# Kernel optimization log

Hardware: AMD Instinct MI355X
Metric: run time of the kernel (lower is better)

## Reference

```python
import jax, jax.numpy as jnp
import numpy as np

D_MODEL = 2048
NUM_HEADS = 16
NUM_KV_HEADS = 4
D_HEAD = D_MODEL // NUM_HEADS  # 128
GROUPS = NUM_HEADS // NUM_KV_HEADS  # 4
ROPE_THETA = 10000.0
EPS = 1e-6


def setup_inputs() -> dict:
    key = jax.random.key(0)
    ks = jax.random.split(key, 7)
    B, S = 2, 2048
    s = 1.0 / np.sqrt(D_MODEL)
    return {
        "qkv": jax.random.normal(ks[0], (B, S, D_MODEL), dtype=jnp.float32),
        "Wq": jax.random.normal(ks[1], (D_MODEL, D_MODEL), dtype=jnp.float32) * s,
        "Wk": jax.random.normal(ks[2], (NUM_KV_HEADS * D_HEAD, D_MODEL), dtype=jnp.float32) * s,
        "Wv": jax.random.normal(ks[3], (NUM_KV_HEADS * D_HEAD, D_MODEL), dtype=jnp.float32) * s,
        "Wo": jax.random.normal(ks[4], (D_MODEL, D_MODEL), dtype=jnp.float32) * s,
        "q_gamma": jnp.ones((D_HEAD,), dtype=jnp.float32),
        "k_gamma": jnp.ones((D_HEAD,), dtype=jnp.float32),
    }


def _rmsnorm(x, gamma):
    # per-head RMSNorm over last dim (d_head)
    var = jnp.mean(jnp.square(x), axis=-1, keepdims=True)
    return x * jax.lax.rsqrt(var + EPS) * gamma


def _rope(x, cos, sin):
    # x: [B, S, H, Dh]; cos/sin: [S, Dh]
    half = x.shape[-1] // 2
    x1, x2 = x[..., :half], x[..., half:]
    rot = jnp.concatenate([-x2, x1], axis=-1)
    return x * cos[None, :, None, :] + rot * sin[None, :, None, :]


def reference(qkv, Wq, Wk, Wv, Wo, q_gamma, k_gamma):
    B, S, D = qkv.shape
    q = jnp.einsum("bsd,ed->bse", qkv, Wq).reshape(B, S, NUM_HEADS, D_HEAD)
    k = jnp.einsum("bsd,ed->bse", qkv, Wk).reshape(B, S, NUM_KV_HEADS, D_HEAD)
    v = jnp.einsum("bsd,ed->bse", qkv, Wv).reshape(B, S, NUM_KV_HEADS, D_HEAD)

    q = _rmsnorm(q, q_gamma)
    k = _rmsnorm(k, k_gamma)

    # RoPE, position_ids = arange(S)
    pos = jnp.arange(S, dtype=jnp.float32)
    inv_freq = 1.0 / (ROPE_THETA ** (jnp.arange(0, D_HEAD, 2, dtype=jnp.float32) / D_HEAD))
    ang = pos[:, None] * inv_freq[None, :]                 # [S, Dh/2]
    cos = jnp.concatenate([jnp.cos(ang), jnp.cos(ang)], axis=-1)  # [S, Dh]
    sin = jnp.concatenate([jnp.sin(ang), jnp.sin(ang)], axis=-1)
    q = _rope(q, cos, sin)
    k = _rope(k, cos, sin)

    # [B, H, S, Dh]
    q = q.transpose(0, 2, 1, 3)
    k = k.transpose(0, 2, 1, 3)
    v = v.transpose(0, 2, 1, 3)
    # GQA: repeat kv heads
    k = jnp.repeat(k, GROUPS, axis=1)
    v = jnp.repeat(v, GROUPS, axis=1)

    scale = 1.0 / np.sqrt(D_HEAD)
    scores = jnp.einsum("bhqd,bhkd->bhqk", q, k) * scale
    causal = jnp.tril(jnp.ones((S, S), dtype=bool))
    scores = jnp.where(causal[None, None], scores, jnp.finfo(scores.dtype).min)
    probs = jax.nn.softmax(scores, axis=-1)
    attended = jnp.einsum("bhqk,bhkd->bhqd", probs, v)     # [B, H, S, Dh]
    attended = attended.transpose(0, 2, 1, 3).reshape(B, S, D)
    return jnp.einsum("bsd,ed->bse", attended, Wo)
```

## Files before the change

kernel.cpp:

```cpp
#include <hip/hip_runtime.h>

#define S_LEN 2048
#define B_SZ 2
#define DMODEL 2048
#define NHEADS 16
#define NKV 4
#define DHEAD 128
#define SCALE 0.08838834764831845f
#define KVB 32

typedef __bf16 bf16x8 __attribute__((ext_vector_type(8)));
typedef __bf16 bf16x4 __attribute__((ext_vector_type(4)));
typedef float f32x4 __attribute__((ext_vector_type(4)));

#define MFMA(a, b, c) __builtin_amdgcn_mfma_f32_16x16x32_bf16(a, b, c, 0, 0, 0)

__device__ __forceinline__ void gload_lds16(const __bf16* g, __bf16* l) {
    __builtin_amdgcn_global_load_lds(
        (const __attribute__((address_space(1))) unsigned int*)g,
        (__attribute__((address_space(3))) unsigned int*)l, 16, 0, 0);
}

__global__ void rope_tables_kernel(float* __restrict__ cosT, float* __restrict__ sinT) {
    int i = blockIdx.x * 256 + threadIdx.x;
    int s = i >> 6, d = i & 63;
    float freq = powf(10000.0f, -(2.0f * (float)d) / 128.0f);
    float ang = (float)s * freq;
    cosT[i] = cosf(ang);
    sinT[i] = sinf(ang);
}

__global__ __launch_bounds__(256) void convert_kernel(
    const float* __restrict__ s0, const float* __restrict__ s1,
    const float* __restrict__ s2, const float* __restrict__ s3,
    const float* __restrict__ s4,
    __bf16* __restrict__ d0, __bf16* __restrict__ d1, __bf16* __restrict__ d2,
    __bf16* __restrict__ d3, __bf16* __restrict__ d4) {
    const float* s;
    __bf16* d;
    int n8;
    switch (blockIdx.y) {
        case 0: s = s0; d = d0; n8 = (B_SZ * S_LEN * DMODEL) / 8; break;
        case 1: s = s1; d = d1; n8 = (DMODEL * DMODEL) / 8; break;
        case 2: s = s2; d = d2; n8 = (NKV * DHEAD * DMODEL) / 8; break;
        case 3: s = s3; d = d3; n8 = (NKV * DHEAD * DMODEL) / 8; break;
        default: s = s4; d = d4; n8 = (DMODEL * DMODEL) / 8; break;
    }
    for (int i = blockIdx.x * 256 + threadIdx.x; i < n8; i += 512 * 256) {
        float4 a = ((const float4*)s)[2 * i];
        float4 b = ((const float4*)s)[2 * i + 1];
        bf16x8 o = {(__bf16)a.x, (__bf16)a.y, (__bf16)a.z, (__bf16)a.w,
                    (__bf16)b.x, (__bf16)b.y, (__bf16)b.z, (__bf16)b.w};
        *(bf16x8*)&d[i * 8] = o;
    }
}

template <int BM>
__device__ __forceinline__ void gemm256(const __bf16* __restrict__ A,
                                        const __bf16* __restrict__ W,
                                        int bm, int bn, int K,
                                        f32x4 (&acc)[BM / 32][4]) {
    constexpr int MI = BM / 32;
    constexpr int ALT = BM / 64;
    __shared__ alignas(16) __bf16 As[2][BM * 64];
    __shared__ alignas(16) __bf16 Bs[2][256 * 64];
    const int tid = threadIdx.x;
    const int lane = tid & 63;
    const int wave = tid >> 6;
    const int lr = lane & 15, lk = lane >> 4;
    const int wr = wave >> 2;
    const int wc = wave & 3;
    const int sRow = lane >> 3;
    const int sCol = 8 * ((lane & 7) ^ sRow);

    auto stageA = [&](int bi, int k0) {
#pragma unroll
        for (int it = 0; it < ALT; ++it) {
            const int row = it * 64 + wave * 8 + sRow;
            gload_lds16(A + (size_t)(bm + row) * K + k0 + sCol,
                        &As[bi][it * 4096 + wave * 512]);
        }
    };
    auto stageB = [&](int bi, int k0) {
#pragma unroll
        for (int it = 0; it < 4; ++it) {
            const int row = it * 64 + wave * 8 + sRow;
            gload_lds16(W + (size_t)(bn + row) * K + k0 + sCol,
                        &Bs[bi][it * 4096 + wave * 512]);
        }
    };

#pragma unroll
    for (int mi = 0; mi < MI; ++mi)
#pragma unroll
        for (int ni = 0; ni < 4; ++ni) acc[mi][ni] = (f32x4){0.f, 0.f, 0.f, 0.f};

    const int NT = K >> 6;
    stageA(0, 0);
    stageB(0, 0);
    stageA(1, 64);
    stageB(1, 64);
    if constexpr (BM == 256) asm volatile("s_waitcnt vmcnt(8)" ::: "memory");
    else                     asm volatile("s_waitcnt vmcnt(6)" ::: "memory");
    __builtin_amdgcn_s_barrier();

    for (int t = 0; t < NT; ++t) {
        const int bi = t & 1;
#pragma unroll
        for (int kk = 0; kk < 2; ++kk) {
            bf16x8 af[MI], bfr[4];
#pragma unroll
            for (int i = 0; i < MI; ++i) {
                const int r = wr * (BM / 2) + i * 16 + lr;
                const int slot = (kk * 4 + lk) ^ (r & 7);
                af[i] = *(const bf16x8*)&As[bi][r * 64 + slot * 8];
            }
#pragma unroll
            for (int i = 0; i < 4; ++i) {
                const int r = wc * 64 + i * 16 + lr;
                const int slot = (kk * 4 + lk) ^ (r & 7);
                bfr[i] = *(const bf16x8*)&Bs[bi][r * 64 + slot * 8];
            }
#pragma unroll
            for (int mi = 0; mi < MI; ++mi)
#pragma unroll
                for (int ni = 0; ni < 4; ++ni)
                    acc[mi][ni] = MFMA(af[mi], bfr[ni], acc[mi][ni]);
        }
        asm volatile("s_waitcnt lgkmcnt(0)" ::: "memory");
        __builtin_amdgcn_sched_barrier(0);
        __builtin_amdgcn_s_barrier();
        if (t + 2 < NT) {
            stageA(bi, (t + 2) * 64);
            stageB(bi, (t + 2) * 64);
        }
        if (t + 1 < NT) {
            if (t + 2 < NT) {
                if constexpr (BM == 256) asm volatile("s_waitcnt vmcnt(8)" ::: "memory");
                else                     asm volatile("s_waitcnt vmcnt(6)" ::: "memory");
            } else {
                asm volatile("s_waitcnt vmcnt(0)" ::: "memory");
            }
            __builtin_amdgcn_s_barrier();
        }
    }
}

__global__ __launch_bounds__(512, 2) void qkv_proj_kernel(
    const __bf16* __restrict__ qkvb, const __bf16* __restrict__ Wq,
    const __bf16* __restrict__ Wk, const __bf16* __restrict__ Wv,
    float* __restrict__ q_tmp, float* __restrict__ k_tmp, float* __restrict__ v_tmp) {
    const int id = (blockIdx.x & 7) * 24 + (blockIdx.x >> 3);
    const int bmi = id / 12, bni = id % 12;
    const int bm = bmi * 256;
    const __bf16* W;
    float* C;
    int ldc, bn;
    if (bni < 8)       { W = Wq; C = q_tmp; ldc = 2048; bn = bni * 256; }
    else if (bni < 10) { W = Wk; C = k_tmp; ldc = 512;  bn = (bni - 8) * 256; }
    else               { W = Wv; C = v_tmp; ldc = 512;  bn = (bni - 10) * 256; }

    f32x4 acc[8][4];
    gemm256<256>(qkvb, W, bm, bn, 2048, acc);

    const int lane = threadIdx.x & 63, wave = threadIdx.x >> 6;
    const int lr = lane & 15, lk = lane >> 4;
    const int wr = wave >> 2, wc = wave & 3;
#pragma unroll
    for (int mi = 0; mi < 8; ++mi)
#pragma unroll
        for (int ni = 0; ni < 4; ++ni)
#pragma unroll
            for (int r = 0; r < 4; ++r) {
                const int row = bm + wr * 128 + mi * 16 + lk * 4 + r;
                const int col = bn + wc * 64 + ni * 16 + lr;
                C[(size_t)row * ldc + col] = acc[mi][ni][r];
            }
}

__global__ __launch_bounds__(512, 2) void out_proj_kernel(
    const __bf16* __restrict__ att, const __bf16* __restrict__ Wo,
    float* __restrict__ out) {
    const int id = (blockIdx.x & 7) * 32 + (blockIdx.x >> 3);
    const int bm = (id >> 3) * 128, bn = (id & 7) * 256;

    f32x4 acc[4][4];
    gemm256<128>(att, Wo, bm, bn, 2048, acc);

    const int lane = threadIdx.x & 63, wave = threadIdx.x >> 6;
    const int lr = lane & 15, lk = lane >> 4;
    const int wr = wave >> 2, wc = wave & 3;
#pragma unroll
    for (int mi = 0; mi < 4; ++mi)
#pragma unroll
        for (int ni = 0; ni < 4; ++ni)
#pragma unroll
            for (int r = 0; r < 4; ++r) {
                const int row = bm + wr * 64 + mi * 16 + lk * 4 + r;
                const int col = bn + wc * 64 + ni * 16 + lr;
                out[(size_t)row * DMODEL + col] = acc[mi][ni][r];
            }
}

__global__ __launch_bounds__(256) void postproc_kernel(
    const float* __restrict__ q_tmp, const float* __restrict__ k_tmp,
    const float* __restrict__ qg, const float* __restrict__ kg,
    const float* __restrict__ cosT, const float* __restrict__ sinT,
    __bf16* __restrict__ qb, __bf16* __restrict__ kb) {
    int bs = blockIdx.x;
    int b = bs >> 11, s = bs & 2047;
    int wave = threadIdx.x >> 6, lane = threadIdx.x & 63;
    float c  = cosT[s * 64 + lane];
    float sn = sinT[s * 64 + lane];
    float g1q = qg[lane], g2q = qg[lane + 64];
    float g1k = kg[lane], g2k = kg[lane + 64];

    for (int h = wave; h < NHEADS; h += 4) {
        const float* row = q_tmp + (size_t)bs * 2048 + h * 128;
        float x1 = row[lane], x2 = row[lane + 64];
        float ss = x1 * x1 + x2 * x2;
#pragma unroll
        for (int m = 1; m < 64; m <<= 1) ss += __shfl_xor(ss, m);
        float rs = rsqrtf(ss * (1.0f / 128.0f) + 1e-6f);
        float n1 = x1 * rs * g1q, n2 = x2 * rs * g2q;
        float y1 = (n1 * c - n2 * sn) * SCALE;
        float y2 = (n2 * c + n1 * sn) * SCALE;
        __bf16* orow = qb + (((size_t)(b * NHEADS + h)) * S_LEN + s) * DHEAD;
        orow[lane] = (__bf16)y1;
        orow[lane + 64] = (__bf16)y2;
    }
    int h = wave;
    if (h < NKV) {
        const float* row = k_tmp + (size_t)bs * 512 + h * 128;
        float x1 = row[lane], x2 = row[lane + 64];
        float ss = x1 * x1 + x2 * x2;
#pragma unroll
        for (int m = 1; m < 64; m <<= 1) ss += __shfl_xor(ss, m);
        float rs = rsqrtf(ss * (1.0f / 128.0f) + 1e-6f);
        float n1 = x1 * rs * g1k, n2 = x2 * rs * g2k;
        float y1 = n1 * c - n2 * sn;
        float y2 = n2 * c + n1 * sn;
        __bf16* orow = kb + (((size_t)(b * NKV + h)) * S_LEN + s) * DHEAD;
        orow[lane] = (__bf16)y1;
        orow[lane + 64] = (__bf16)y2;
    }
}

__global__ __launch_bounds__(256) void v_transpose_kernel(
    const float* __restrict__ v_tmp, __bf16* __restrict__ vt) {
    int bkv = blockIdx.x;
    int b = bkv >> 2, kvh = bkv & 3;
    int s0 = blockIdx.y * 64, d0 = blockIdx.z * 64;
    __shared__ float tile[64][65];
#pragma unroll
    for (int i = 0; i < 16; ++i) {
        int idx = threadIdx.x + i * 256;
        int r = idx >> 6, cc = idx & 63;
        tile[r][cc] = v_tmp[((size_t)(b * S_LEN) + s0 + r) * 512 + kvh * 128 + d0 + cc];
    }
    __syncthreads();
#pragma unroll
    for (int i = 0; i < 16; ++i) {
        int idx = threadIdx.x + i * 256;
        int r = idx >> 6, cc = idx & 63;
        vt[((size_t)bkv * DHEAD + d0 + r) * S_LEN + s0 + cc] = (__bf16)tile[cc][r];
    }
}

__global__ __launch_bounds__(256, 2) void flash_kernel(
    const __bf16* __restrict__ qb, const __bf16* __restrict__ kb,
    const __bf16* __restrict__ vt, __bf16* __restrict__ att) {
    __shared__ alignas(16) __bf16 K_lds[2][32 * 128];
    __shared__ alignas(16) __bf16 V_lds[2][128 * 32];
    __shared__ alignas(16) __bf16 p_lds[4][16][40];

    const int bh = blockIdx.x;
    const int b = bh >> 4, h = bh & 15, kv = h >> 2;
    const int j = blockIdx.y;
    const int lane = threadIdx.x & 63, wave = threadIdx.x >> 6;
    const int lr = lane & 15, lk = lane >> 4;

    const int qloB = j * 64 + wave * 16;
    const int qhiB = (31 - j) * 64 + wave * 16;
    const int ntL  = ((qloB + 15) >> 5) + 1;
    const int ntHw = ((qhiB + 15) >> 5) + 1;
    const int ntH  = 64 - 2 * j;

    const __bf16* Qp = qb + ((size_t)(b * NHEADS + h)) * S_LEN * DHEAD;
    const __bf16* Kp = kb + ((size_t)(b * NKV + kv)) * S_LEN * DHEAD;
    const __bf16* Vt = vt + ((size_t)(b * NKV + kv)) * DHEAD * S_LEN;

    bf16x8 qlo[4], qhi[4];
#pragma unroll
    for (int f = 0; f < 4; ++f) {
        qlo[f] = *(const bf16x8*)&Qp[(size_t)(qloB + lr) * DHEAD + f * 32 + lk * 8];
        qhi[f] = *(const bf16x8*)&Qp[(size_t)(qhiB + lr) * DHEAD + f * 32 + lk * 8];
    }

    const int c0 = 2 * wave;
    const int l4 = lane >> 4, l15 = lane & 15;
    const int l2 = lane >> 2, l3 = lane & 3;
    const int vcol = ((l3 ^ (l2 & 3)) << 3);

    auto stage = [&](int bufi, int t) {
        const int k0s = t * KVB;
#pragma unroll
        for (int i = 0; i < 2; ++i) {
            const int c = c0 + i;
            const int rK = c * 4 + l4;
            const int kcol = ((l15 ^ (rK & 7)) << 3);
            gload_lds16(Kp + (size_t)(k0s + rK) * DHEAD + kcol, &K_lds[bufi][c * 512]);
            const int rV = c * 16 + l2;
            gload_lds16(Vt + (size_t)rV * S_LEN + k0s + vcol, &V_lds[bufi][c * 512]);
        }
    };

    f32x4 accL[8] = {}, accH[8] = {};
    float lsumL[4] = {0.f, 0.f, 0.f, 0.f}, lsumH[4] = {0.f, 0.f, 0.f, 0.f};
    const int swzK = (lr & 7) << 4;
    const int swzV = (lr & 3) << 4;

    auto frag_step = [&](const bf16x8 (&qf)[4], int qbase, f32x4 (&acc)[8],
                         float (&lsum)[4], const bf16x8 (&kf)[8],
                         const bf16x8 (&vf)[8], int k0) {
        f32x4 sc[2] = {};
#pragma unroll
        for (int kk = 0; kk < 2; ++kk)
#pragma unroll
            for (int f = 0; f < 4; ++f)
                sc[kk] = MFMA(qf[f], kf[kk * 4 + f], sc[kk]);
        asm volatile("s_waitcnt lgkmcnt(0)" ::: "memory");
#pragma unroll
        for (int r = 0; r < 4; ++r) {
            const int qr = qbase + lk * 4 + r;
            float s0 = sc[0][r], s1 = sc[1][r];
            if (k0 + lr > qr) s0 = -1e30f;
            if (k0 + 16 + lr > qr) s1 = -1e30f;
            float p0 = __expf(s0), p1 = __expf(s1);
            lsum[r] += p0 + p1;
            p_lds[wave][lk * 4 + r][lr] = (__bf16)p0;
            p_lds[wave][lk * 4 + r][lr + 16] = (__bf16)p1;
        }
        asm volatile("s_waitcnt lgkmcnt(0)" ::: "memory");
        bf16x8 pf = *(const bf16x8*)&p_lds[wave][lr][lk * 8];
#pragma unroll
        for (int nf = 0; nf < 8; ++nf)
            acc[nf] = MFMA(pf, vf[nf], acc[nf]);
    };

    int cur = 0;
    stage(0, 0);
    __syncthreads();
    for (int t = 0; t < ntH; ++t) {
        if (t + 1 < ntH) stage(cur ^ 1, t + 1);
        const int k0 = t * KVB;
        bf16x8 kf[8], vf[8];
#pragma unroll
        for (int kk = 0; kk < 2; ++kk)
#pragma unroll
            for (int f = 0; f < 4; ++f) {
                const int cb = (f * 64 + lk * 16) ^ swzK;
                kf[kk * 4 + f] =
                    *(const bf16x8*)((const char*)&K_lds[cur][(kk * 16 + lr) * 128] + cb);
            }
#pragma unroll
        for (int nf = 0; nf < 8; ++nf) {
            const int cb = (lk * 16) ^ swzV;
            vf[nf] = *(const bf16x8*)((const char*)&V_lds[cur][(nf * 16 + lr) * 32] + cb);
        }
        if (t < ntHw) frag_step(qhi, qhiB, accH, lsumH, kf, vf, k0);
        if (t < ntL)  frag_step(qlo, qloB, accL, lsumL, kf, vf, k0);
        __syncthreads();
        cur ^= 1;
    }

#pragma unroll
    for (int r = 0; r < 4; ++r) {
#pragma unroll
        for (int m = 1; m < 16; m <<= 1) {
            lsumL[r] += __shfl_xor(lsumL[r], m);
            lsumH[r] += __shfl_xor(lsumH[r], m);
        }
    }
#pragma unroll
    for (int nf = 0; nf < 8; ++nf)
#pragma unroll
        for (int r = 0; r < 4; ++r) {
            int qrL = qloB + lk * 4 + r;
            int qrH = qhiB + lk * 4 + r;
            att[((size_t)(b * S_LEN) + qrL) * DMODEL + h * DHEAD + nf * 16 + lr] =
                (__bf16)(accL[nf][r] / lsumL[r]);
            att[((size_t)(b * S_LEN) + qrH) * DMODEL + h * DHEAD + nf * 16 + lr] =
                (__bf16)(accH[nf][r] / lsumH[r]);
        }
}

extern "C" void kernel_launch(void* const* d_in, const int* in_sizes, int n_in,
                              void* d_out, int out_size, void* d_ws, size_t ws_size,
                              hipStream_t stream) {
    const float* qkv = (const float*)d_in[0];
    const float* Wq  = (const float*)d_in[1];
    const float* Wk  = (const float*)d_in[2];
    const float* Wv  = (const float*)d_in[3];
    const float* Wo  = (const float*)d_in[4];
    const float* qg  = (const float*)d_in[5];
    const float* kg  = (const float*)d_in[6];
    float* out = (float*)d_out;

    size_t off = 0;
    char* wsb = (char*)d_ws;
    auto alloc = [&](size_t n) {
        char* p = wsb + off;
        off += (n + 255) & ~(size_t)255;
        return (void*)p;
    };
    const size_t M = (size_t)B_SZ * S_LEN;
    float* cosT  = (float*)alloc((size_t)S_LEN * 64 * 4);
    float* sinT  = (float*)alloc((size_t)S_LEN * 64 * 4);
    float* q_tmp = (float*)alloc(M * 2048 * 4);
    float* k_tmp = (float*)alloc(M * 512 * 4);
    float* v_tmp = (float*)alloc(M * 512 * 4);
    __bf16* qb   = (__bf16*)alloc((size_t)B_SZ * NHEADS * S_LEN * DHEAD * 2);
    __bf16* kb   = (__bf16*)alloc((size_t)B_SZ * NKV * S_LEN * DHEAD * 2);
    __bf16* vt   = (__bf16*)alloc((size_t)B_SZ * NKV * DHEAD * S_LEN * 2);
    __bf16* att  = (__bf16*)alloc(M * DMODEL * 2);
    __bf16* wo_b = (__bf16*)alloc((size_t)DMODEL * DMODEL * 2);
    __bf16* qkv_b = att;
    __bf16* wq_b  = qb;
    __bf16* wk_b  = vt;
    __bf16* wv_b  = wk_b + (size_t)NKV * DHEAD * DMODEL;

    rope_tables_kernel<<<(S_LEN * 64) / 256, 256, 0, stream>>>(cosT, sinT);
    convert_kernel<<<dim3(512, 5), 256, 0, stream>>>(qkv, Wq, Wk, Wv, Wo,
                                                     qkv_b, wq_b, wk_b, wv_b, wo_b);
    qkv_proj_kernel<<<192, 512, 0, stream>>>(qkv_b, wq_b, wk_b, wv_b,
                                             q_tmp, k_tmp, v_tmp);
    postproc_kernel<<<dim3(M), 256, 0, stream>>>(q_tmp, k_tmp, qg, kg, cosT, sinT, qb, kb);
    v_transpose_kernel<<<dim3(B_SZ * NKV, S_LEN / 64, DHEAD / 64), 256, 0, stream>>>(v_tmp, vt);
    flash_kernel<<<dim3(B_SZ * NHEADS, 16), 256, 0, stream>>>(qb, kb, vt, att);
    out_proj_kernel<<<256, 512, 0, stream>>>(att, wo_b, out);
}
```

Before: 211.5 us.

## Fuse RMSNorm, RoPE and V transpose into QKV projection epilogue

Measured after the change: 195.3 us. 7.6% less time.

```diff
diff --git a/kernel.cpp b/kernel.cpp
--- a/kernel.cpp
+++ b/kernel.cpp
@@ -59,11 +59,12 @@
 __device__ __forceinline__ void gemm256(const __bf16* __restrict__ A,
                                         const __bf16* __restrict__ W,
                                         int bm, int bn, int K,
-                                        f32x4 (&acc)[BM / 32][4]) {
+                                        f32x4 (&acc)[BM / 32][4],
+                                        __bf16* arena) {
     constexpr int MI = BM / 32;
     constexpr int ALT = BM / 64;
-    __shared__ alignas(16) __bf16 As[2][BM * 64];
-    __shared__ alignas(16) __bf16 Bs[2][256 * 64];
+    __bf16* As = arena;
+    __bf16* Bs = arena + 2 * BM * 64;
     const int tid = threadIdx.x;
     const int lane = tid & 63;
     const int wave = tid >> 6;
@@ -78,7 +79,7 @@
         for (int it = 0; it < ALT; ++it) {
             const int row = it * 64 + wave * 8 + sRow;
             gload_lds16(A + (size_t)(bm + row) * K + k0 + sCol,
-                        &As[bi][it * 4096 + wave * 512]);
+                        As + bi * BM * 64 + it * 4096 + wave * 512);
         }
     };
     auto stageB = [&](int bi, int k0) {
@@ -86,7 +87,7 @@
         for (int it = 0; it < 4; ++it) {
             const int row = it * 64 + wave * 8 + sRow;
             gload_lds16(W + (size_t)(bn + row) * K + k0 + sCol,
-                        &Bs[bi][it * 4096 + wave * 512]);
+                        Bs + bi * 16384 + it * 4096 + wave * 512);
         }
     };
 
@@ -113,13 +114,13 @@
             for (int i = 0; i < MI; ++i) {
                 const int r = wr * (BM / 2) + i * 16 + lr;
                 const int slot = (kk * 4 + lk) ^ (r & 7);
-                af[i] = *(const bf16x8*)&As[bi][r * 64 + slot * 8];
+                af[i] = *(const bf16x8*)&As[bi * BM * 64 + r * 64 + slot * 8];
             }
 #pragma unroll
             for (int i = 0; i < 4; ++i) {
                 const int r = wc * 64 + i * 16 + lr;
                 const int slot = (kk * 4 + lk) ^ (r & 7);
-                bfr[i] = *(const bf16x8*)&Bs[bi][r * 64 + slot * 8];
+                bfr[i] = *(const bf16x8*)&Bs[bi * 16384 + r * 64 + slot * 8];
             }
 #pragma unroll
             for (int mi = 0; mi < MI; ++mi)
@@ -149,43 +150,138 @@
 __global__ __launch_bounds__(512, 2) void qkv_proj_kernel(
     const __bf16* __restrict__ qkvb, const __bf16* __restrict__ Wq,
     const __bf16* __restrict__ Wk, const __bf16* __restrict__ Wv,
-    float* __restrict__ q_tmp, float* __restrict__ k_tmp, float* __restrict__ v_tmp) {
+    const float* __restrict__ qg, const float* __restrict__ kg,
+    const float* __restrict__ cosT, const float* __restrict__ sinT,
+    __bf16* __restrict__ qb, __bf16* __restrict__ kb, __bf16* __restrict__ vt) {
+    __shared__ alignas(16) __bf16 arena[4 * 256 * 64];
     const int id = (blockIdx.x & 7) * 24 + (blockIdx.x >> 3);
     const int bmi = id / 12, bni = id % 12;
     const int bm = bmi * 256;
     const __bf16* W;
-    float* C;
-    int ldc, bn;
-    if (bni < 8)       { W = Wq; C = q_tmp; ldc = 2048; bn = bni * 256; }
-    else if (bni < 10) { W = Wk; C = k_tmp; ldc = 512;  bn = (bni - 8) * 256; }
-    else               { W = Wv; C = v_tmp; ldc = 512;  bn = (bni - 10) * 256; }
+    int bn;
+    if (bni < 8)       { W = Wq; bn = bni * 256; }
+    else if (bni < 10) { W = Wk; bn = (bni - 8) * 256; }
+    else               { W = Wv; bn = (bni - 10) * 256; }
 
     f32x4 acc[8][4];
-    gemm256<256>(qkvb, W, bm, bn, 2048, acc);
-
-    const int lane = threadIdx.x & 63, wave = threadIdx.x >> 6;
+    gemm256<256>(qkvb, W, bm, bn, 2048, acc, arena);
+
+    const int tid = threadIdx.x;
+    const int lane = tid & 63, wave = tid >> 6;
     const int lr = lane & 15, lk = lane >> 4;
     const int wr = wave >> 2, wc = wave & 3;
-#pragma unroll
-    for (int mi = 0; mi < 8; ++mi)
-#pragma unroll
-        for (int ni = 0; ni < 4; ++ni)
+    const int dc0 = (wc & 1) * 64;
+
+    if (bni < 10) {
+        const bool isQ = (bni < 8);
+        const float* gamma = isQ ? qg : kg;
+        const float scl = isQ ? SCALE : 1.0f;
+        const int hh = (isQ ? bni * 2 : (bni - 8) * 2) + (wc >> 1);
+        const int nh = isQ ? NHEADS : NKV;
+        __bf16* outb = isQ ? qb : kb;
+        float g[4];
+#pragma unroll
+        for (int ni = 0; ni < 4; ++ni) g[ni] = gamma[dc0 + ni * 16 + lr];
+
+        float* xbuf = (float*)arena;
+        float* ssbuf = (float*)((char*)arena + 70 * 1024);
+
+        float rs[8][4];
+#pragma unroll
+        for (int mi = 0; mi < 8; ++mi)
 #pragma unroll
             for (int r = 0; r < 4; ++r) {
-                const int row = bm + wr * 128 + mi * 16 + lk * 4 + r;
-                const int col = bn + wc * 64 + ni * 16 + lr;
-                C[(size_t)row * ldc + col] = acc[mi][ni][r];
-            }
+                float ss = 0.f;
+#pragma unroll
+                for (int ni = 0; ni < 4; ++ni) ss += acc[mi][ni][r] * acc[mi][ni][r];
+                ss += __shfl_xor(ss, 1);
+                ss += __shfl_xor(ss, 2);
+                ss += __shfl_xor(ss, 4);
+                ss += __shfl_xor(ss, 8);
+                if (lr == 0) ssbuf[wc * 256 + wr * 128 + mi * 16 + lk * 4 + r] = ss;
+            }
+        __syncthreads();
+#pragma unroll
+        for (int mi = 0; mi < 8; ++mi)
+#pragma unroll
+            for (int r = 0; r < 4; ++r) {
+                const int rowl = wr * 128 + mi * 16 + lk * 4 + r;
+                const float tot = ssbuf[wc * 256 + rowl] + ssbuf[(wc ^ 1) * 256 + rowl];
+                rs[mi][r] = rsqrtf(tot * (1.0f / 128.0f) + 1e-6f) * scl;
+            }
+        __syncthreads();
+
+#pragma unroll
+        for (int ch = 0; ch < 4; ++ch) {
+            float y[2][4][4];
+#pragma unroll
+            for (int m2 = 0; m2 < 2; ++m2)
+#pragma unroll
+                for (int ni = 0; ni < 4; ++ni)
+#pragma unroll
+                    for (int r = 0; r < 4; ++r) {
+                        const int mi = ch * 2 + m2;
+                        y[m2][ni][r] = acc[mi][ni][r] * rs[mi][r] * g[ni];
+                        xbuf[tid * 33 + m2 * 16 + ni * 4 + r] = y[m2][ni][r];
+                    }
+            __syncthreads();
+            float yp[2][4][4];
+#pragma unroll
+            for (int m2 = 0; m2 < 2; ++m2)
+#pragma unroll
+                for (int ni = 0; ni < 4; ++ni)
+#pragma unroll
+                    for (int r = 0; r < 4; ++r)
+                        yp[m2][ni][r] = xbuf[(tid ^ 64) * 33 + m2 * 16 + ni * 4 + r];
+#pragma unroll
+            for (int m2 = 0; m2 < 2; ++m2)
+#pragma unroll
+                for (int r = 0; r < 4; ++r) {
+                    const int mi = ch * 2 + m2;
+                    const int gm = bm + wr * 128 + mi * 16 + lk * 4 + r;
+                    const int bb = gm >> 11, s = gm & 2047;
+                    const float* ct = cosT + s * 64;
+                    const float* st = sinT + s * 64;
+                    __bf16* orow = outb + (((size_t)(bb * nh + hh)) * S_LEN + s) * DHEAD;
+#pragma unroll
+                    for (int ni = 0; ni < 4; ++ni) {
+                        const int dd = ni * 16 + lr;
+                        const float c = ct[dd], sn = st[dd];
+                        const float own = y[m2][ni][r], par = yp[m2][ni][r];
+                        const float o = (wc & 1) ? (own * c + par * sn)
+                                                 : (own * c - par * sn);
+                        orow[dc0 + dd] = (__bf16)o;
+                    }
+                }
+            __syncthreads();
+        }
+    } else {
+        const int kvh = (bni - 10) * 2 + (wc >> 1);
+#pragma unroll
+        for (int mi = 0; mi < 8; ++mi) {
+            const int gm = bm + wr * 128 + mi * 16 + lk * 4;
+            const int bb = gm >> 11, s0 = gm & 2047;
+            __bf16* vbase = vt + ((size_t)(bb * NKV + kvh)) * DHEAD * S_LEN;
+#pragma unroll
+            for (int ni = 0; ni < 4; ++ni) {
+                const int d = dc0 + ni * 16 + lr;
+                bf16x4 pk = {(__bf16)acc[mi][ni][0], (__bf16)acc[mi][ni][1],
+                             (__bf16)acc[mi][ni][2], (__bf16)acc[mi][ni][3]};
+                *(bf16x4*)&vbase[(size_t)d * S_LEN + s0] = pk;
+            }
+        }
+    }
 }
 
 __global__ __launch_bounds__(512, 2) void out_proj_kernel(
     const __bf16* __restrict__ att, const __bf16* __restrict__ Wo,
     float* __restrict__ out) {
+    __shared__ alignas(16) __bf16 arena[2 * 128 * 64 + 2 * 256 * 64];
     const int id = (blockIdx.x & 7) * 32 + (blockIdx.x >> 3);
     const int bm = (id >> 3) * 128, bn = (id & 7) * 256;
 
     f32x4 acc[4][4];
-    gemm256<128>(att, Wo, bm, bn, 2048, acc);
+    gemm256<128>(att, Wo, bm, bn, 2048, acc, arena);
 
     const int lane = threadIdx.x & 63, wave = threadIdx.x >> 6;
     const int lr = lane & 15, lk = lane >> 4;
@@ -200,71 +296,6 @@
                 const int col = bn + wc * 64 + ni * 16 + lr;
                 out[(size_t)row * DMODEL + col] = acc[mi][ni][r];
             }
-}
-
-__global__ __launch_bounds__(256) void postproc_kernel(
-    const float* __restrict__ q_tmp, const float* __restrict__ k_tmp,
-    const float* __restrict__ qg, const float* __restrict__ kg,
-    const float* __restrict__ cosT, const float* __restrict__ sinT,
-    __bf16* __restrict__ qb, __bf16* __restrict__ kb) {
-    int bs = blockIdx.x;
-    int b = bs >> 11, s = bs & 2047;
-    int wave = threadIdx.x >> 6, lane = threadIdx.x & 63;
-    float c  = cosT[s * 64 + lane];
-    float sn = sinT[s * 64 + lane];
-    float g1q = qg[lane], g2q = qg[lane + 64];
-    float g1k = kg[lane], g2k = kg[lane + 64];
-
-    for (int h = wave; h < NHEADS; h += 4) {
-        const float* row = q_tmp + (size_t)bs * 2048 + h * 128;
-        float x1 = row[lane], x2 = row[lane + 64];
-        float ss = x1 * x1 + x2 * x2;
-#pragma unroll
-        for (int m = 1; m < 64; m <<= 1) ss += __shfl_xor(ss, m);
-        float rs = rsqrtf(ss * (1.0f / 128.0f) + 1e-6f);
-        float n1 = x1 * rs * g1q, n2 = x2 * rs * g2q;
-        float y1 = (n1 * c - n2 * sn) * SCALE;
-        float y2 = (n2 * c + n1 * sn) * SCALE;
-        __bf16* orow = qb + (((size_t)(b * NHEADS + h)) * S_LEN + s) * DHEAD;
-        orow[lane] = (__bf16)y1;
-        orow[lane + 64] = (__bf16)y2;
-    }
-    int h = wave;
-    if (h < NKV) {
-        const float* row = k_tmp + (size_t)bs * 512 + h * 128;
-        float x1 = row[lane], x2 = row[lane + 64];
-        float ss = x1 * x1 + x2 * x2;
-#pragma unroll
-        for (int m = 1; m < 64; m <<= 1) ss += __shfl_xor(ss, m);
-        float rs = rsqrtf(ss * (1.0f / 128.0f) + 1e-6f);
-        float n1 = x1 * rs * g1k, n2 = x2 * rs * g2k;
-        float y1 = n1 * c - n2 * sn;
-        float y2 = n2 * c + n1 * sn;
-        __bf16* orow = kb + (((size_t)(b * NKV + h)) * S_LEN + s) * DHEAD;
-        orow[lane] = (__bf16)y1;
-        orow[lane + 64] = (__bf16)y2;
-    }
-}
-
-__global__ __launch_bounds__(256) void v_transpose_kernel(
-    const float* __restrict__ v_tmp, __bf16* __restrict__ vt) {
-    int bkv = blockIdx.x;
-    int b = bkv >> 2, kvh = bkv & 3;
-    int s0 = blockIdx.y * 64, d0 = blockIdx.z * 64;
-    __shared__ float tile[64][65];
-#pragma unroll
-    for (int i = 0; i < 16; ++i) {
-        int idx = threadIdx.x + i * 256;
-        int r = idx >> 6, cc = idx & 63;
-        tile[r][cc] = v_tmp[((size_t)(b * S_LEN) + s0 + r) * 512 + kvh * 128 + d0 + cc];
-    }
-    __syncthreads();
-#pragma unroll
-    for (int i = 0; i < 16; ++i) {
-        int idx = threadIdx.x + i * 256;
-        int r = idx >> 6, cc = idx & 63;
-        vt[((size_t)bkv * DHEAD + d0 + r) * S_LEN + s0 + cc] = (__bf16)tile[cc][r];
-    }
 }
 
 __global__ __launch_bounds__(256, 2) void flash_kernel(
@@ -324,11 +355,13 @@
                          float (&lsum)[4], const bf16x8 (&kf)[8],
                          const bf16x8 (&vf)[8], int k0) {
         f32x4 sc[2] = {};
+        __builtin_amdgcn_s_setprio(1);
 #pragma unroll
         for (int kk = 0; kk < 2; ++kk)
 #pragma unroll
             for (int f = 0; f < 4; ++f)
                 sc[kk] = MFMA(qf[f], kf[kk * 4 + f], sc[kk]);
+        __builtin_amdgcn_s_setprio(0);
         asm volatile("s_waitcnt lgkmcnt(0)" ::: "memory");
 #pragma unroll
         for (int r = 0; r < 4; ++r) {
@@ -343,9 +376,11 @@
         }
         asm volatile("s_waitcnt lgkmcnt(0)" ::: "memory");
         bf16x8 pf = *(const bf16x8*)&p_lds[wave][lr][lk * 8];
+        __builtin_amdgcn_s_setprio(1);
 #pragma unroll
         for (int nf = 0; nf < 8; ++nf)
             acc[nf] = MFMA(pf, vf[nf], acc[nf]);
+        __builtin_amdgcn_s_setprio(0);
     };
 
     int cur = 0;
@@ -415,28 +450,23 @@
         return (void*)p;
     };
     const size_t M = (size_t)B_SZ * S_LEN;
-    float* cosT  = (float*)alloc((size_t)S_LEN * 64 * 4);
-    float* sinT  = (float*)alloc((size_t)S_LEN * 64 * 4);
-    float* q_tmp = (float*)alloc(M * 2048 * 4);
-    float* k_tmp = (float*)alloc(M * 512 * 4);
-    float* v_tmp = (float*)alloc(M * 512 * 4);
-    __bf16* qb   = (__bf16*)alloc((size_t)B_SZ * NHEADS * S_LEN * DHEAD * 2);
-    __bf16* kb   = (__bf16*)alloc((size_t)B_SZ * NKV * S_LEN * DHEAD * 2);
-    __bf16* vt   = (__bf16*)alloc((size_t)B_SZ * NKV * DHEAD * S_LEN * 2);
-    __bf16* att  = (__bf16*)alloc(M * DMODEL * 2);
-    __bf16* wo_b = (__bf16*)alloc((size_t)DMODEL * DMODEL * 2);
-    __bf16* qkv_b = att;
-    __bf16* wq_b  = qb;
-    __bf16* wk_b  = vt;
-    __bf16* wv_b  = wk_b + (size_t)NKV * DHEAD * DMODEL;
+    float* cosT   = (float*)alloc((size_t)S_LEN * 64 * 4);
+    float* sinT   = (float*)alloc((size_t)S_LEN * 64 * 4);
+    __bf16* qb    = (__bf16*)alloc((size_t)B_SZ * NHEADS * S_LEN * DHEAD * 2);
+    __bf16* kb    = (__bf16*)alloc((size_t)B_SZ * NKV * S_LEN * DHEAD * 2);
+    __bf16* vt    = (__bf16*)alloc((size_t)B_SZ * NKV * DHEAD * S_LEN * 2);
+    __bf16* att   = (__bf16*)alloc(M * DMODEL * 2);
+    __bf16* qkv_b = (__bf16*)alloc(M * DMODEL * 2);
+    __bf16* wq_b  = (__bf16*)alloc((size_t)DMODEL * DMODEL * 2);
+    __bf16* wk_b  = (__bf16*)alloc((size_t)NKV * DHEAD * DMODEL * 2);
+    __bf16* wv_b  = (__bf16*)alloc((size_t)NKV * DHEAD * DMODEL * 2);
+    __bf16* wo_b  = (__bf16*)alloc((size_t)DMODEL * DMODEL * 2);
 
     rope_tables_kernel<<<(S_LEN * 64) / 256, 256, 0, stream>>>(cosT, sinT);
     convert_kernel<<<dim3(512, 5), 256, 0, stream>>>(qkv, Wq, Wk, Wv, Wo,
                                                      qkv_b, wq_b, wk_b, wv_b, wo_b);
     qkv_proj_kernel<<<192, 512, 0, stream>>>(qkv_b, wq_b, wk_b, wv_b,
-                                             q_tmp, k_tmp, v_tmp);
-    postproc_kernel<<<dim3(M), 256, 0, stream>>>(q_tmp, k_tmp, qg, kg, cosT, sinT, qb, kb);
-    v_transpose_kernel<<<dim3(B_SZ * NKV, S_LEN / 64, DHEAD / 64), 256, 0, stream>>>(v_tmp, vt);
+                                             qg, kg, cosT, sinT, qb, kb, vt);
     flash_kernel<<<dim3(B_SZ * NHEADS, 16), 256, 0, stream>>>(qb, kb, vt, att);
     out_proj_kernel<<<256, 512, 0, stream>>>(att, wo_b, out);
 }
```
